# Performance work log

Measured on AMD Instinct MI355X. Metric: run time of the kernel, lower is better.

Reference implementation:

```python
import jax, jax.numpy as jnp
import numpy as np

N = 50000      # nodes
E = 800000     # edges (before self-loops)
F_IN = 256     # num_features
NCLS = 8       # num_classes


def setup_inputs() -> dict:
    key = jax.random.key(0)
    ks = jax.random.split(key, 24)
    s = 0.05
    rn = lambda k, shape: jax.random.normal(k, shape, jnp.float32) * s
    return {
        "x": jax.random.normal(ks[0], (N, F_IN), jnp.float32),
        "edge_index": jax.random.randint(ks[1], (2, E), 0, N, dtype=jnp.int32),
        "w1": rn(ks[2], (F_IN, 512)), "b1": jnp.zeros((512,), jnp.float32),
        "w2": rn(ks[3], (512, 256)), "b2": jnp.zeros((256,), jnp.float32),
        "w3": rn(ks[4], (256, 128)), "b3": jnp.zeros((128,), jnp.float32),
        "wc1": rn(ks[5], (128, 256)), "as1": rn(ks[6], (4, 64)), "ad1": rn(ks[7], (4, 64)), "bc1": jnp.zeros((256,), jnp.float32),
        "wc2": rn(ks[8], (256, 128)), "as2": rn(ks[9], (4, 32)), "ad2": rn(ks[10], (4, 32)), "bc2": jnp.zeros((128,), jnp.float32),
        "wc3": rn(ks[11], (128, 8)), "as3": rn(ks[12], (1, 8)), "ad3": rn(ks[13], (1, 8)), "bc3": jnp.zeros((8,), jnp.float32),
    }


def _gat_conv(x, src, dst, W, att_src, att_dst, bias, heads, out_ch, concat):
    """PyG GATConv (eval mode): gather -> LeakyReLU attn -> segment softmax -> scatter-add."""
    n = x.shape[0]
    h = (x @ W).reshape(n, heads, out_ch)                  # [N,H,C]
    a_src = jnp.einsum('nhc,hc->nh', h, att_src)           # [N,H]
    a_dst = jnp.einsum('nhc,hc->nh', h, att_dst)           # [N,H]
    e = jax.nn.leaky_relu(a_src[src] + a_dst[dst], 0.2)    # [E,H]
    # numerically-stable softmax over edges grouped by destination node
    m = jax.ops.segment_max(e, dst, num_segments=n)        # [N,H]
    m = jnp.where(jnp.isfinite(m), m, 0.0)
    ex = jnp.exp(e - m[dst])
    denom = jax.ops.segment_sum(ex, dst, num_segments=n)   # [N,H]
    alpha = ex / jnp.maximum(denom[dst], 1e-16)            # [E,H]
    out = jax.ops.segment_sum(h[src] * alpha[:, :, None], dst, num_segments=n)  # [N,H,C]
    out = out.reshape(n, heads * out_ch) if concat else out.mean(axis=1)
    return out + bias


def reference(x, edge_index, w1, b1, w2, b2, w3, b3,
              wc1, as1, ad1, bc1, wc2, as2, ad2, bc2, wc3, as3, ad3, bc3):
    n = x.shape[0]
    # add self-loops (PyG GATConv default)
    loops = jnp.arange(n, dtype=edge_index.dtype)
    src = jnp.concatenate([edge_index[0], loops])
    dst = jnp.concatenate([edge_index[1], loops])

    h = jax.nn.relu(x @ w1 + b1)
    h = jax.nn.relu(h @ w2 + b2)
    h = jax.nn.relu(h @ w3 + b3)          # [N,128]; dropout inactive in eval

    h = jax.nn.elu(_gat_conv(h, src, dst, wc1, as1, ad1, bc1, 4, 64, True))   # [N,256]
    h = jax.nn.elu(_gat_conv(h, src, dst, wc2, as2, ad2, bc2, 4, 32, True))   # [N,128]
    out = _gat_conv(h, src, dst, wc3, as3, ad3, bc3, 1, NCLS, False)          # [N,8]
    return out
```

## Files before the change

### kernel.cpp

```cpp
#include <hip/hip_runtime.h>
#include <hip/hip_bf16.h>

#define NODES 50000
#define E0    800000
#define ETOT  (E0 + NODES)

typedef short  short8  __attribute__((ext_vector_type(8)));
typedef unsigned short ushort8 __attribute__((ext_vector_type(8)));
typedef float  f32x4   __attribute__((ext_vector_type(4)));
typedef __hip_bfloat16 bf16;

__device__ __forceinline__ float bfbits(unsigned short u) {
    return __uint_as_float(((unsigned)u) << 16);
}
__device__ __forceinline__ float lrelu(float x) { return x > 0.f ? x : 0.2f * x; }
__device__ __forceinline__ float pick4(float4 v, int i) {
    float r = (i == 0) ? v.x : (i == 1) ? v.y : (i == 2) ? v.z : v.w;
    return r;
}

__device__ __forceinline__ void gload16(const void* g, unsigned short* l) {
    __builtin_amdgcn_global_load_lds(
        (const __attribute__((address_space(1))) unsigned int*)g,
        (__attribute__((address_space(3))) unsigned int*)l,
        16, 0, 0);
}

__global__ void f32_to_bf16(const float* __restrict__ in, bf16* __restrict__ out, int n4)
{
    int i = blockIdx.x * 256 + threadIdx.x;
    if (i >= n4) return;
    float4 v = *(const float4*)(in + (size_t)i * 4);
    bf16* o = out + (size_t)i * 4;
    o[0] = __float2bfloat16(v.x); o[1] = __float2bfloat16(v.y);
    o[2] = __float2bfloat16(v.z); o[3] = __float2bfloat16(v.w);
}

__device__ __forceinline__ void wtr(const float* w, bf16* wt, int K, int N, int t)
{
    int k = t / N, n = t % N;
    wt[(size_t)n * K + k] = __float2bfloat16(w[t]);
}

__global__ void w_transpose_all(
    const float* w1, const float* w2, const float* w3,
    const float* wc1, const float* wc2,
    bf16* w1T, bf16* w2T, bf16* w3T, bf16* wc1T, bf16* wc2T)
{
    int t = blockIdx.x * 256 + threadIdx.x;
    if      (t < 131072)  wtr(w1,  w1T,  256, 512, t);
    else if (t < 262144)  wtr(w2,  w2T,  512, 256, t - 131072);
    else if (t < 294912)  wtr(w3,  w3T,  256, 128, t - 262144);
    else if (t < 327680)  wtr(wc1, wc1T, 128, 256, t - 294912);
    else if (t < 360448)  wtr(wc2, wc2T, 256, 128, t - 327680);
}

template<int SLC>
__global__ __launch_bounds__(256) void mfma_gemm(
    const bf16* __restrict__ A, const bf16* __restrict__ Bt,
    const float* __restrict__ bias, bf16* __restrict__ C,
    int M, int N, int K, int relu,
    const float* __restrict__ att_s, const float* __restrict__ att_d,
    float* __restrict__ aSo, float* __restrict__ aDo)
{
    __shared__ union {
        unsigned short AB[2][2][128 * 32];
        unsigned short Cs[128 * 136];
    } lds;

    const int tid  = threadIdx.x;
    const int wave = tid >> 6, lane = tid & 63;
    const int bm = blockIdx.y * 128, bn = blockIdx.x * 128;
    const int wr = (wave >> 1) * 64, wc = (wave & 1) * 64;
    const int lr = lane & 15, kg = lane >> 4;

    const int srow0 = tid >> 2, sko = (tid & 3) * 8;
    const int srow1 = srow0 + 64;
    int arow0 = bm + srow0; if (arow0 >= M) arow0 = M - 1;
    int arow1 = bm + srow1; if (arow1 >= M) arow1 = M - 1;
    const unsigned short* gA0 = (const unsigned short*)A + (size_t)arow0 * K + sko;
    const unsigned short* gA1 = (const unsigned short*)A + (size_t)arow1 * K + sko;
    const unsigned short* gB0 = (const unsigned short*)Bt + (size_t)(bn + srow0) * K + sko;
    const unsigned short* gB1 = (const unsigned short*)Bt + (size_t)(bn + srow1) * K + sko;

    f32x4 acc[4][4];
    #pragma unroll
    for (int m = 0; m < 4; m++)
        #pragma unroll
        for (int n = 0; n < 4; n++)
            #pragma unroll
            for (int j = 0; j < 4; j++) acc[m][n][j] = 0.f;

    const int nk = K >> 5;

    #define STAGE(buf, kk)                                              \
        gload16(gA0 + ((kk) << 5), &lds.AB[buf][0][tid * 8]);           \
        gload16(gA1 + ((kk) << 5), &lds.AB[buf][0][(tid + 256) * 8]);   \
        gload16(gB0 + ((kk) << 5), &lds.AB[buf][1][tid * 8]);           \
        gload16(gB1 + ((kk) << 5), &lds.AB[buf][1][(tid + 256) * 8]);

    STAGE(0, 0)
    __syncthreads();

    int cur = 0;
    for (int k = 0; k < nk; k++) {
        if (k + 1 < nk) {
            STAGE(cur ^ 1, k + 1)
        }
        short8 af[4], bfr[4];
        #pragma unroll
        for (int m = 0; m < 4; m++)
            af[m] = *(const short8*)&lds.AB[cur][0][(wr + m * 16 + lr) * 32 + kg * 8];
        #pragma unroll
        for (int n = 0; n < 4; n++)
            bfr[n] = *(const short8*)&lds.AB[cur][1][(wc + n * 16 + lr) * 32 + kg * 8];
        #pragma unroll
        for (int m = 0; m < 4; m++)
            #pragma unroll
            for (int n = 0; n < 4; n++)
                acc[m][n] = __builtin_amdgcn_mfma_f32_16x16x32_bf16(af[m], bfr[n], acc[m][n], 0, 0, 0);
        __syncthreads();
        cur ^= 1;
    }
    #undef STAGE

    #pragma unroll
    for (int m = 0; m < 4; m++) {
        #pragma unroll
        for (int n = 0; n < 4; n++) {
            const int col = wc + n * 16 + lr;
            const float bv = bias ? bias[bn + col] : 0.f;
            #pragma unroll
            for (int j = 0; j < 4; j++) {
                const int r = wr + m * 16 + kg * 4 + j;
                float v = acc[m][n][j] + bv;
                if (relu) v = fmaxf(v, 0.f);
                lds.Cs[r * 136 + col] = __bfloat16_as_ushort(__float2bfloat16(v));
            }
        }
    }
    __syncthreads();
    {
        const int row = tid >> 1, hf2 = tid & 1;
        const int gr = bm + row;
        if (gr < M) {
            const unsigned short* srcp = &lds.Cs[row * 136 + hf2 * 64];
            unsigned short* dstp = (unsigned short*)C + (size_t)gr * N + bn + hf2 * 64;
            ushort8 chunk[8];
            #pragma unroll
            for (int i = 0; i < 8; i++) chunk[i] = *(const ushort8*)(srcp + i * 8);
            #pragma unroll
            for (int i = 0; i < 8; i++) *(ushort8*)(dstp + i * 8) = chunk[i];
            if constexpr (SLC > 0) {
                constexpr int NH = 64 / SLC;
                const int seg0 = bn + hf2 * 64;
                #pragma unroll
                for (int hh = 0; hh < NH; hh++) {
                    const int head = (seg0 >> (SLC == 64 ? 6 : 5)) + hh;
                    const float* asv = att_s + head * SLC;
                    const float* adv = att_d + head * SLC;
                    float vs = 0.f, vd = 0.f;
                    #pragma unroll
                    for (int i = 0; i < SLC; i++) {
                        const int idx = hh * SLC + i;
                        float f = bfbits(chunk[idx >> 3][idx & 7]);
                        vs = fmaf(f, asv[i], vs);
                        vd = fmaf(f, adv[i], vd);
                    }
                    aSo[gr * 4 + head] = vs;
                    aDo[gr * 4 + head] = vd;
                }
            }
        }
    }
}

__global__ void gemm_n8_scores(const bf16* __restrict__ A, const float* __restrict__ B,
                               float* __restrict__ C, int M, int K,
                               const float* __restrict__ as3, const float* __restrict__ ad3,
                               float* __restrict__ aS, float* __restrict__ aD)
{
    int t = blockIdx.x * 256 + threadIdx.x;
    int m = t >> 3, n = t & 7;
    if (m >= M) return;
    float s = 0.f;
    const ushort8* A8 = (const ushort8*)((const unsigned short*)A + (size_t)m * K);
    #pragma unroll 4
    for (int k8 = 0; k8 < K / 8; k8++) {
        ushort8 a = A8[k8];
        #pragma unroll
        for (int j = 0; j < 8; j++)
            s += bfbits(a[j]) * B[(k8 * 8 + j) * 8 + n];
    }
    C[t] = s;
    float vs = s * as3[n], vd = s * ad3[n];
    #pragma unroll
    for (int off = 1; off < 8; off <<= 1) {
        vs += __shfl_xor(vs, off);
        vd += __shfl_xor(vd, off);
    }
    if (n == 0) { aS[m] = vs; aD[m] = vd; }
}

__device__ __forceinline__ void edge_sd(int e, int& s, int& d,
                                        const int* __restrict__ src,
                                        const int* __restrict__ dst) {
    if (e < E0) { s = src[e]; d = dst[e]; } else { s = e - E0; d = s; }
}

__global__ void deg_hist(const int* __restrict__ src, const int* __restrict__ dst,
                         int* __restrict__ deg)
{
    int e = blockIdx.x * 256 + threadIdx.x;
    if (e >= ETOT) return;
    int s, d; edge_sd(e, s, d, src, dst);
    atomicAdd(&deg[d], 1);
}

__global__ void scan_block(const int* __restrict__ deg, int* __restrict__ ptr,
                           int* __restrict__ bsum, int n)
{
    __shared__ int sm[256];
    int t = threadIdx.x, i = blockIdx.x * 256 + t;
    int v = (i < n) ? deg[i] : 0;
    sm[t] = v; __syncthreads();
    #pragma unroll
    for (int off = 1; off < 256; off <<= 1) {
        int x = (t >= off) ? sm[t - off] : 0;
        __syncthreads();
        sm[t] += x; __syncthreads();
    }
    if (i < n) ptr[i] = sm[t] - v;
    if (t == 255) bsum[blockIdx.x] = sm[255];
}

__global__ void scan_bsum(int* __restrict__ bsum, int nb)
{
    __shared__ int sm[256];
    int t = threadIdx.x;
    int v = (t < nb) ? bsum[t] : 0;
    sm[t] = v; __syncthreads();
    #pragma unroll
    for (int off = 1; off < 256; off <<= 1) {
        int x = (t >= off) ? sm[t - off] : 0;
        __syncthreads();
        sm[t] += x; __syncthreads();
    }
    if (t < nb) bsum[t] = sm[t] - v;
}

__global__ void scan_add(int* __restrict__ ptr, const int* __restrict__ bsum, int n)
{
    int i = blockIdx.x * 256 + threadIdx.x;
    if (i < n) ptr[i] += bsum[blockIdx.x];
    if (i == 0) ptr[n] = ETOT;
}

__global__ void csr_fill(const int* __restrict__ src, const int* __restrict__ dst,
                         const int* __restrict__ ptr, int* __restrict__ cursor,
                         int* __restrict__ csr)
{
    int e = blockIdx.x * 256 + threadIdx.x;
    if (e >= ETOT) return;
    int s, d; edge_sd(e, s, d, src, dst);
    int pos = ptr[d] + atomicAdd(&cursor[d], 1);
    csr[pos] = s;
}

template<int C>
__global__ __launch_bounds__(256) void gat_wave(
    const bf16* __restrict__ hf, const float* __restrict__ aSv,
    const float* __restrict__ aDv, const int* __restrict__ ptr,
    const int* __restrict__ csr, const float* __restrict__ bias,
    bf16* __restrict__ out, int elu)
{
    constexpr int W   = 4 * C;
    constexpr int LPE = W / 8;
    constexpr int EPI = 64 / LPE;
    constexpr int CS  = (C == 64) ? 3 : 2;

    __shared__ int   ls[4][64];
    __shared__ float lwT[4][4][68];

    const int wv = threadIdx.x >> 6, lane = threadIdx.x & 63;
    const int d = blockIdx.x * 4 + wv;
    if (d >= NODES) return;
    const int beg = ptr[d], end = ptr[d + 1];

    const int lsub  = lane % LPE;
    const int h_own = lsub >> CS;
    const int ch0   = lsub * 8;

    const float4 aDd = *(const float4*)&aDv[d * 4];
    float4 den4 = {0.f, 0.f, 0.f, 0.f};
    float acc[8] = {};

    for (int tbeg = beg; tbeg < end; tbeg += 64) {
        const int nval = min(64, end - tbeg);

        if (lane < nval) {
            int s = csr[tbeg + lane];
            float4 a = *(const float4*)&aSv[s * 4];
            float4 ex;
            ex.x = __expf(lrelu(a.x + aDd.x));
            ex.y = __expf(lrelu(a.y + aDd.y));
            ex.z = __expf(lrelu(a.z + aDd.z));
            ex.w = __expf(lrelu(a.w + aDd.w));
            den4.x += ex.x; den4.y += ex.y; den4.z += ex.z; den4.w += ex.w;
            ls[wv][lane] = s;
            lwT[wv][0][lane] = ex.x;
            lwT[wv][1][lane] = ex.y;
            lwT[wv][2][lane] = ex.z;
            lwT[wv][3][lane] = ex.w;
        }

        for (int j = lane / LPE; j < nval; j += EPI) {
            const int   sj  = ls[wv][j];
            const float wgt = lwT[wv][h_own][j];
            ushort8 r = *(const ushort8*)((const unsigned short*)hf + (size_t)sj * W + ch0);
            #pragma unroll
            for (int k = 0; k < 8; k++) acc[k] += wgt * bfbits(r[k]);
        }
    }

    #pragma unroll
    for (int off = 32; off; off >>= 1) {
        den4.x += __shfl_xor(den4.x, off);
        den4.y += __shfl_xor(den4.y, off);
        den4.z += __shfl_xor(den4.z, off);
        den4.w += __shfl_xor(den4.w, off);
    }
    #pragma unroll
    for (int k = 0; k < 8; k++) {
        #pragma unroll
        for (int off = LPE; off < 64; off <<= 1)
            acc[k] += __shfl_xor(acc[k], off);
    }

    if (lane < LPE) {
        const float deno = fmaxf(pick4({den4.x, den4.y, den4.z, den4.w}, h_own), 1e-16f);
        const float rden = 1.f / deno;
        ushort8 o;
        #pragma unroll
        for (int k = 0; k < 8; k++) {
            float v = acc[k] * rden + bias[ch0 + k];
            if (elu) v = v > 0.f ? v : expm1f(v);
            o[k] = (unsigned short)(__bfloat16_as_ushort(__float2bfloat16(v)));
        }
        *(ushort8*)((unsigned short*)out + (size_t)d * W + ch0) = o;
    }
}

__global__ void gat3_onepass(const float* __restrict__ hc3, const float* __restrict__ aS,
                             const float* __restrict__ aD, const int* __restrict__ ptr,
                             const int* __restrict__ csr, const float* __restrict__ bias,
                             float* __restrict__ out)
{
    int t = blockIdx.x * 256 + threadIdx.x;
    int d = t >> 3, c = t & 7;
    if (d >= NODES) return;
    const int beg = ptr[d], end = ptr[d + 1];
    const float aDd = aD[d];
    float acc = 0.f, den = 0.f;
    for (int i = beg; i < end; i++) {
        int s = csr[i];
        float ex = __expf(lrelu(aS[s] + aDd));
        den += ex;
        acc += ex * hc3[s * 8 + c];
    }
    out[d * 8 + c] = acc / fmaxf(den, 1e-16f) + bias[c];
}

extern "C" void kernel_launch(void* const* d_in, const int* in_sizes, int n_in,
                              void* d_out, int out_size, void* d_ws, size_t ws_size,
                              hipStream_t stream)
{
    const float* x   = (const float*)d_in[0];
    const int*   ei  = (const int*)d_in[1];
    const float* w1  = (const float*)d_in[2];  const float* b1  = (const float*)d_in[3];
    const float* w2  = (const float*)d_in[4];  const float* b2  = (const float*)d_in[5];
    const float* w3  = (const float*)d_in[6];  const float* b3  = (const float*)d_in[7];
    const float* wc1 = (const float*)d_in[8];  const float* as1 = (const float*)d_in[9];
    const float* ad1 = (const float*)d_in[10]; const float* bc1 = (const float*)d_in[11];
    const float* wc2 = (const float*)d_in[12]; const float* as2 = (const float*)d_in[13];
    const float* ad2 = (const float*)d_in[14]; const float* bc2 = (const float*)d_in[15];
    const float* wc3 = (const float*)d_in[16]; const float* as3 = (const float*)d_in[17];
    const float* ad3 = (const float*)d_in[18]; const float* bc3 = (const float*)d_in[19];

    const int* srcv = ei;
    const int* dstv = ei + E0;

    char* ws = (char*)d_ws;
    bf16*  xb    = (bf16*)(ws + 0);
    bf16*  h2b   = (bf16*)(ws + 0);
    bf16*  h1b   = (bf16*)(ws + 25600000);
    bf16*  hc1b  = (bf16*)(ws + 25600000);
    bf16*  out1b = (bf16*)(ws + 51200000);
    bf16*  h3b   = (bf16*)(ws + 76800000);
    bf16*  hc2b  = (bf16*)(ws + 76800000);
    bf16*  out2b = (bf16*)(ws + 89600000);
    float* hc3   = (float*)(ws + 102400000);
    float* aS    = (float*)(ws + 104000000);
    float* aD    = (float*)(ws + 104800000);
    int*   ptr   = (int*)  (ws + 105600000);
    int*   deg   = (int*)  (ws + 105900000);
    int*   curs  = (int*)  (ws + 106100000);
    int*   bsum  = (int*)  (ws + 106300000);
    int*   csr   = (int*)  (ws + 106400000);
    bf16*  w1T   = (bf16*)(ws + 110000000);
    bf16*  w2T   = (bf16*)(ws + 110300000);
    bf16*  w3T   = (bf16*)(ws + 110600000);
    bf16*  wc1T  = (bf16*)(ws + 110700000);
    bf16*  wc2T  = (bf16*)(ws + 110800000);
    if (ws_size < (size_t)196000000) return;

    float* outf = (float*)d_out;
    dim3 blk(256);
    const int NB_SCAN = (NODES + 255) / 256;

    (void)hipMemsetAsync(deg, 0, (size_t)400000, stream);
    deg_hist<<<(ETOT + 255)/256, blk, 0, stream>>>(srcv, dstv, deg);
    scan_block<<<NB_SCAN, blk, 0, stream>>>(deg, ptr, bsum, NODES);
    scan_bsum<<<1, blk, 0, stream>>>(bsum, NB_SCAN);
    scan_add<<<NB_SCAN, blk, 0, stream>>>(ptr, bsum, NODES);
    csr_fill<<<(ETOT + 255)/256, blk, 0, stream>>>(srcv, dstv, ptr, curs, csr);

    f32_to_bf16<<<(NODES*256/4 + 255)/256, blk, 0, stream>>>(x, xb, NODES*256/4);
    w_transpose_all<<<(360448 + 255)/256, blk, 0, stream>>>(w1, w2, w3, wc1, wc2,
                                                            w1T, w2T, w3T, wc1T, wc2T);

    const int gy = (NODES + 127) / 128;
    mfma_gemm<0><<<dim3(4, gy), blk, 0, stream>>>(xb,  w1T, b1, h1b, NODES, 512, 256, 1,
                                                  nullptr, nullptr, nullptr, nullptr);
    mfma_gemm<0><<<dim3(2, gy), blk, 0, stream>>>(h1b, w2T, b2, h2b, NODES, 256, 512, 1,
                                                  nullptr, nullptr, nullptr, nullptr);
    mfma_gemm<0><<<dim3(1, gy), blk, 0, stream>>>(h2b, w3T, b3, h3b, NODES, 128, 256, 1,
                                                  nullptr, nullptr, nullptr, nullptr);

    mfma_gemm<64><<<dim3(2, gy), blk, 0, stream>>>(h3b, wc1T, nullptr, hc1b, NODES, 256, 128, 0,
                                                   as1, ad1, aS, aD);
    gat_wave<64><<<(NODES + 3)/4, blk, 0, stream>>>(hc1b, aS, aD, ptr, csr, bc1, out1b, 1);

    mfma_gemm<32><<<dim3(1, gy), blk, 0, stream>>>(out1b, wc2T, nullptr, hc2b, NODES, 128, 256, 0,
                                                   as2, ad2, aS, aD);
    gat_wave<32><<<(NODES + 3)/4, blk, 0, stream>>>(hc2b, aS, aD, ptr, csr, bc2, out2b, 1);

    gemm_n8_scores<<<(NODES*8 + 255)/256, blk, 0, stream>>>(out2b, wc3, hc3, NODES, 128,
                                                            as3, ad3, aS, aD);
    gat3_onepass<<<(NODES*8 + 255)/256, blk, 0, stream>>>(hc3, aS, aD, ptr, csr, bc3, outf);
}
```

Baseline: 420.5 us.

## Precompute per-edge attention weights in separate kernel and widen per-lane channels to 16

Adds a destination array to the CSR build and a new edge_weights kernel that computes exp(leaky_relu(aS[s]+aD[d])) for every edge ahead of each GAT aggregation. The aggregation kernels then read precomputed weights instead of gathering aS and computing exp inline. Separately, gat_wave now has each lane handle 16 channels with two 16-byte loads instead of 8, halving lanes per edge and doubling edges processed per iteration. This adds three extra kernel launches plus extra memory traffic (csrd write, ew write and read of ~850K float4), in exchange for moving the scattered aS gathers out of the latency-bound aggregation loop.

```diff
diff --git a/kernel.cpp b/kernel.cpp
--- a/kernel.cpp
+++ b/kernel.cpp
@@ -258,26 +258,49 @@
 
 __global__ void csr_fill(const int* __restrict__ src, const int* __restrict__ dst,
                          const int* __restrict__ ptr, int* __restrict__ cursor,
-                         int* __restrict__ csr)
+                         int* __restrict__ csr, int* __restrict__ csrd)
 {
     int e = blockIdx.x * 256 + threadIdx.x;
     if (e >= ETOT) return;
     int s, d; edge_sd(e, s, d, src, dst);
     int pos = ptr[d] + atomicAdd(&cursor[d], 1);
     csr[pos] = s;
+    csrd[pos] = d;
+}
+
+template<int H>
+__global__ void edge_weights(const float* __restrict__ aS, const float* __restrict__ aD,
+                             const int* __restrict__ csr, const int* __restrict__ csrd,
+                             float* __restrict__ ew)
+{
+    int i = blockIdx.x * 256 + threadIdx.x;
+    if (i >= ETOT) return;
+    int s = csr[i], d = csrd[i];
+    if constexpr (H == 4) {
+        float4 a = ((const float4*)aS)[s];
+        float4 b = ((const float4*)aD)[d];
+        float4 e;
+        e.x = __expf(lrelu(a.x + b.x));
+        e.y = __expf(lrelu(a.y + b.y));
+        e.z = __expf(lrelu(a.z + b.z));
+        e.w = __expf(lrelu(a.w + b.w));
+        ((float4*)ew)[i] = e;
+    } else {
+        ew[i] = __expf(lrelu(aS[s] + aD[d]));
+    }
 }
 
 template<int C>
 __global__ __launch_bounds__(256) void gat_wave(
-    const bf16* __restrict__ hf, const float* __restrict__ aSv,
-    const float* __restrict__ aDv, const int* __restrict__ ptr,
-    const int* __restrict__ csr, const float* __restrict__ bias,
-    bf16* __restrict__ out, int elu)
+    const bf16* __restrict__ hf, const float* __restrict__ ew,
+    const int* __restrict__ ptr, const int* __restrict__ csr,
+    const float* __restrict__ bias, bf16* __restrict__ out, int elu)
 {
     constexpr int W   = 4 * C;
-    constexpr int LPE = W / 8;
+    constexpr int CPL = 16;
+    constexpr int LPE = W / CPL;
     constexpr int EPI = 64 / LPE;
-    constexpr int CS  = (C == 64) ? 3 : 2;
+    constexpr int HS  = (C == 64) ? 2 : 1;
 
     __shared__ int   ls[4][64];
     __shared__ float lwT[4][4][68];
@@ -288,26 +311,19 @@
     const int beg = ptr[d], end = ptr[d + 1];
 
     const int lsub  = lane % LPE;
-    const int h_own = lsub >> CS;
-    const int ch0   = lsub * 8;
-
-    const float4 aDd = *(const float4*)&aDv[d * 4];
+    const int h_own = lsub >> HS;
+    const int ch0   = lsub * CPL;
+
     float4 den4 = {0.f, 0.f, 0.f, 0.f};
-    float acc[8] = {};
+    float acc[CPL] = {};
 
     for (int tbeg = beg; tbeg < end; tbeg += 64) {
         const int nval = min(64, end - tbeg);
 
         if (lane < nval) {
-            int s = csr[tbeg + lane];
-            float4 a = *(const float4*)&aSv[s * 4];
-            float4 ex;
-            ex.x = __expf(lrelu(a.x + aDd.x));
-            ex.y = __expf(lrelu(a.y + aDd.y));
-            ex.z = __expf(lrelu(a.z + aDd.z));
-            ex.w = __expf(lrelu(a.w + aDd.w));
+            ls[wv][lane] = csr[tbeg + lane];
+            float4 ex = ((const float4*)ew)[tbeg + lane];
             den4.x += ex.x; den4.y += ex.y; den4.z += ex.z; den4.w += ex.w;
-            ls[wv][lane] = s;
             lwT[wv][0][lane] = ex.x;
             lwT[wv][1][lane] = ex.y;
             lwT[wv][2][lane] = ex.z;
@@ -317,9 +333,14 @@
         for (int j = lane / LPE; j < nval; j += EPI) {
             const int   sj  = ls[wv][j];
             const float wgt = lwT[wv][h_own][j];
-            ushort8 r = *(const ushort8*)((const unsigned short*)hf + (size_t)sj * W + ch0);
-            #pragma unroll
-            for (int k = 0; k < 8; k++) acc[k] += wgt * bfbits(r[k]);
+            const unsigned short* rp = (const unsigned short*)hf + (size_t)sj * W + ch0;
+            ushort8 r0 = *(const ushort8*)rp;
+            ushort8 r1 = *(const ushort8*)(rp + 8);
+            #pragma unroll
+            for (int k = 0; k < 8; k++) {
+                acc[k]     += wgt * bfbits(r0[k]);
+                acc[k + 8] += wgt * bfbits(r1[k]);
+            }
         }
     }
 
@@ -331,7 +352,7 @@
         den4.w += __shfl_xor(den4.w, off);
     }
     #pragma unroll
-    for (int k = 0; k < 8; k++) {
+    for (int k = 0; k < CPL; k++) {
         #pragma unroll
         for (int off = LPE; off < 64; off <<= 1)
             acc[k] += __shfl_xor(acc[k], off);
@@ -340,33 +361,37 @@
     if (lane < LPE) {
         const float deno = fmaxf(pick4({den4.x, den4.y, den4.z, den4.w}, h_own), 1e-16f);
         const float rden = 1.f / deno;
-        ushort8 o;
+        ushort8 o0, o1;
         #pragma unroll
         for (int k = 0; k < 8; k++) {
-            float v = acc[k] * rden + bias[ch0 + k];
-            if (elu) v = v > 0.f ? v : expm1f(v);
-            o[k] = (unsigned short)(__bfloat16_as_ushort(__float2bfloat16(v)));
-        }
-        *(ushort8*)((unsigned short*)out + (size_t)d * W + ch0) = o;
-    }
-}
-
-__global__ void gat3_onepass(const float* __restrict__ hc3, const float* __restrict__ aS,
-                             const float* __restrict__ aD, const int* __restrict__ ptr,
-                             const int* __restrict__ csr, const float* __restrict__ bias,
-                             float* __restrict__ out)
+            float v0 = acc[k] * rden + bias[ch0 + k];
+            float v1 = acc[k + 8] * rden + bias[ch0 + 8 + k];
+            if (elu) {
+                v0 = v0 > 0.f ? v0 : expm1f(v0);
+                v1 = v1 > 0.f ? v1 : expm1f(v1);
+            }
+            o0[k] = (unsigned short)__bfloat16_as_ushort(__float2bfloat16(v0));
+            o1[k] = (unsigned short)__bfloat16_as_ushort(__float2bfloat16(v1));
+        }
+        unsigned short* op = (unsigned short*)out + (size_t)d * W + ch0;
+        *(ushort8*)op = o0;
+        *(ushort8*)(op + 8) = o1;
+    }
+}
+
+__global__ void gat3_onepass(const float* __restrict__ hc3, const float* __restrict__ ew,
+                             const int* __restrict__ ptr, const int* __restrict__ csr,
+                             const float* __restrict__ bias, float* __restrict__ out)
 {
     int t = blockIdx.x * 256 + threadIdx.x;
     int d = t >> 3, c = t & 7;
     if (d >= NODES) return;
     const int beg = ptr[d], end = ptr[d + 1];
-    const float aDd = aD[d];
     float acc = 0.f, den = 0.f;
     for (int i = beg; i < end; i++) {
-        int s = csr[i];
-        float ex = __expf(lrelu(aS[s] + aDd));
+        float ex = ew[i];
         den += ex;
-        acc += ex * hc3[s * 8 + c];
+        acc += ex * hc3[csr[i] * 8 + c];
     }
     out[d * 8 + c] = acc / fmaxf(den, 1e-16f) + bias[c];
 }
@@ -412,18 +437,21 @@
     bf16*  w3T   = (bf16*)(ws + 110600000);
     bf16*  wc1T  = (bf16*)(ws + 110700000);
     bf16*  wc2T  = (bf16*)(ws + 110800000);
+    int*   csrd  = (int*)  (ws + 113000000);
+    float* ew    = (float*)(ws + 120000000);
     if (ws_size < (size_t)196000000) return;
 
     float* outf = (float*)d_out;
     dim3 blk(256);
     const int NB_SCAN = (NODES + 255) / 256;
+    const int NB_E = (ETOT + 255) / 256;
 
     (void)hipMemsetAsync(deg, 0, (size_t)400000, stream);
-    deg_hist<<<(ETOT + 255)/256, blk, 0, stream>>>(srcv, dstv, deg);
+    deg_hist<<<NB_E, blk, 0, stream>>>(srcv, dstv, deg);
     scan_block<<<NB_SCAN, blk, 0, stream>>>(deg, ptr, bsum, NODES);
     scan_bsum<<<1, blk, 0, stream>>>(bsum, NB_SCAN);
     scan_add<<<NB_SCAN, blk, 0, stream>>>(ptr, bsum, NODES);
-    csr_fill<<<(ETOT + 255)/256, blk, 0, stream>>>(srcv, dstv, ptr, curs, csr);
+    csr_fill<<<NB_E, blk, 0, stream>>>(srcv, dstv, ptr, curs, csr, csrd);
 
     f32_to_bf16<<<(NODES*256/4 + 255)/256, blk, 0, stream>>>(x, xb, NODES*256/4);
     w_transpose_all<<<(360448 + 255)/256, blk, 0, stream>>>(w1, w2, w3, wc1, wc2,
@@ -439,13 +467,16 @@
 
     mfma_gemm<64><<<dim3(2, gy), blk, 0, stream>>>(h3b, wc1T, nullptr, hc1b, NODES, 256, 128, 0,
                                                    as1, ad1, aS, aD);
-    gat_wave<64><<<(NODES + 3)/4, blk, 0, stream>>>(hc1b, aS, aD, ptr, csr, bc1, out1b, 1);
+    edge_weights<4><<<NB_E, blk, 0, stream>>>(aS, aD, csr, csrd, ew);
+    gat_wave<64><<<(NODES + 3)/4, blk, 0, stream>>>(hc1b, ew, ptr, csr, bc1, out1b, 1);
 
     mfma_gemm<32><<<dim3(1, gy), blk, 0, stream>>>(out1b, wc2T, nullptr, hc2b, NODES, 128, 256, 0,
                                                    as2, ad2, aS, aD);
-    gat_wave<32><<<(NODES + 3)/4, blk, 0, stream>>>(hc2b, aS, aD, ptr, csr, bc2, out2b, 1);
+    edge_weights<4><<<NB_E, blk, 0, stream>>>(aS, aD, csr, csrd, ew);
+    gat_wave<32><<<(NODES + 3)/4, blk, 0, stream>>>(hc2b, ew, ptr, csr, bc2, out2b, 1);
 
     gemm_n8_scores<<<(NODES*8 + 255)/256, blk, 0, stream>>>(out2b, wc3, hc3, NODES, 128,
                                                             as3, ad3, aS, aD);
-    gat3_onepass<<<(NODES*8 + 255)/256, blk, 0, stream>>>(hc3, aS, aD, ptr, csr, bc3, outf);
-}
+    edge_weights<1><<<NB_E, blk, 0, stream>>>(aS, aD, csr, csrd, ew);
+    gat3_onepass<<<(NODES*8 + 255)/256, blk, 0, stream>>>(hc3, ew, ptr, csr, bc3, outf);
+}
```

Result: slower. 450.2 us (+7.1%).
